# Performance work log

Measured on AMD Instinct MI355X. Metric: run time of the kernel, lower is better.

The kernel has to match this reference:

```python
import jax, jax.numpy as jnp
import numpy as np

N_NODES = 100000
N_EDGES = 1600000
IN_CH = 512
HID_CH = 256
OUT_CH = 32
K = 10


def setup_inputs() -> dict:
    key = jax.random.key(0)
    k_x, k_e, k_w1, k_b1, k_w2, k_b2 = jax.random.split(key, 6)
    x = jax.random.normal(k_x, (N_NODES, IN_CH), dtype=jnp.float32)
    edge_index = jax.random.randint(k_e, (2, N_EDGES), 0, N_NODES, dtype=jnp.int64)
    s1 = 1.0 / np.sqrt(IN_CH)
    s2 = 1.0 / np.sqrt(HID_CH)
    W1 = jax.random.uniform(k_w1, (IN_CH, HID_CH), jnp.float32, -s1, s1)
    b1 = jax.random.uniform(k_b1, (HID_CH,), jnp.float32, -s1, s1)
    W2 = jax.random.uniform(k_w2, (HID_CH, OUT_CH), jnp.float32, -s2, s2)
    b2 = jax.random.uniform(k_b2, (OUT_CH,), jnp.float32, -s2, s2)
    gamma = jnp.ones((K + 1,), jnp.float32) / (K + 1)
    return {"x": x, "edge_index": edge_index, "W1": W1, "b1": b1,
            "W2": W2, "b2": b2, "gamma": gamma}


def reference(x, edge_index, W1, b1, W2, b2, gamma):
    # MLP (dropout is identity in eval mode)
    h = jax.nn.relu(x @ W1 + b1) @ W2 + b2  # [N, out]
    row, col = edge_index[0], edge_index[1]
    # symmetric normalization: deg over destination nodes (col)
    deg = jax.ops.segment_sum(jnp.ones((N_EDGES,), h.dtype), col,
                              num_segments=N_NODES)
    deg_inv_sqrt = jnp.where(deg > 0, jax.lax.rsqrt(jnp.maximum(deg, 1.0)), 0.0)
    norm = (deg_inv_sqrt[row] * deg_inv_sqrt[col])[:, None]  # [E, 1]
    out = gamma[0] * h
    h_k = h
    for k in range(1, K + 1):
        # one hop: gather source feats, scale, scatter-add to destinations
        h_k = jax.ops.segment_sum(norm * h_k[row], col, num_segments=N_NODES)
        out = out + gamma[k] * h_k
    return out
```

## Files before the change

kernel.cpp:

```cpp
#include <hip/hip_runtime.h>
#include <hip/hip_bf16.h>

#define NN    100000
#define NE    1600000
#define INCH  512
#define HIDCH 256
#define OUTCH 32
#define KHOPS 10
#define NEPAD (NE + 3 * NN)
#define NBKT  8
#define BDIV  12500
#define BCAP  204800
#define EPB_A 8192
#define EPB_B 2048

typedef __attribute__((ext_vector_type(8))) short short8;
typedef __attribute__((ext_vector_type(4))) float f32x4;

#define GLOAD_LDS16(gsrc, ldst) \
  __builtin_amdgcn_global_load_lds((const __attribute__((address_space(1))) void*)(gsrc), \
                                   (__attribute__((address_space(3))) void*)(ldst), 16, 0, 0)

constexpr size_t ws_align(size_t x) { return (x + 255) & ~(size_t)255; }
constexpr size_t USZ = ws_align((size_t)(NN + 1) * 32 * 2);
constexpr size_t USH = USZ / 2;
constexpr size_t OFF_U0    = 0;
constexpr size_t OFF_W1TH  = OFF_U0    + 11 * USZ;
constexpr size_t OFF_W1TL  = OFF_W1TH  + ws_align((size_t)HIDCH*INCH*2);
constexpr size_t OFF_W2TH  = OFF_W1TL  + ws_align((size_t)HIDCH*INCH*2);
constexpr size_t OFF_W2TL  = OFF_W2TH  + ws_align((size_t)OUTCH*HIDCH*2);
constexpr size_t OFF_DEG   = OFF_W2TL  + ws_align((size_t)OUTCH*HIDCH*2);
constexpr size_t OFF_DIS   = OFF_DEG   + ws_align((size_t)NN*4);
constexpr size_t OFF_RP    = OFF_DIS   + ws_align((size_t)NN*4);
constexpr size_t OFF_CUR   = OFF_RP    + ws_align((size_t)(NN+1)*4);
constexpr size_t OFF_NAP   = OFF_CUR   + ws_align((size_t)NN*4);
constexpr size_t OFF_POSV  = OFF_NAP   + ws_align((size_t)NN*4);
constexpr size_t OFF_PDGP  = OFF_POSV  + ws_align((size_t)NN*4);
constexpr size_t OFF_D2P   = OFF_PDGP  + ws_align((size_t)NN*4);
constexpr size_t OFF_DSQP  = OFF_D2P   + ws_align((size_t)NN*4);
constexpr size_t OFF_CSR   = OFF_DSQP  + ws_align((size_t)NN*4);
constexpr size_t OFF_PART  = OFF_CSR   + ws_align((size_t)NEPAD*4);
constexpr size_t OFF_OFFS  = OFF_PART  + ws_align(512);
constexpr size_t OFF_BCNT  = OFF_OFFS  + ws_align(512);
constexpr size_t OFF_BINH  = OFF_BCNT  + ws_align(32);
constexpr size_t OFF_BINO  = OFF_BINH  + ws_align(256);
constexpr size_t OFF_BINC  = OFF_BINO  + ws_align(256);
constexpr size_t OFF_EPK8  = OFF_BINC  + ws_align(256);

__device__ __forceinline__ unsigned short bf16_rne(float f) {
  unsigned int u = __float_as_uint(f);
  u += 0x7fffu + ((u >> 16) & 1u);
  return (unsigned short)(u >> 16);
}
__device__ __forceinline__ float bf16_to_f32(unsigned short h) {
  return __uint_as_float(((unsigned int)h) << 16);
}
__device__ __forceinline__ float bflo(unsigned int w) {
  return __uint_as_float(w << 16);
}
__device__ __forceinline__ float bfhi(unsigned int w) {
  return __uint_as_float(w & 0xffff0000u);
}

__global__ __launch_bounds__(256) void k_bucket(const int* __restrict__ ei,
                                                int* __restrict__ deg,
                                                int* __restrict__ bcnt,
                                                int2* __restrict__ epk8) {
  __shared__ int hist[NBKT], rbase[NBKT], lcur[NBKT];
  const int t = threadIdx.x;
  const int e0 = blockIdx.x * EPB_A;
  if (t < NBKT) hist[t] = 0;
  __syncthreads();
  for (int i = t; i < EPB_A; i += 256) {
    int e = e0 + i;
    if (e < NE) {
      int c = ei[NE + e];
      atomicAdd(&deg[c], 1);
      atomicAdd(&hist[c / BDIV], 1);
    }
  }
  __syncthreads();
  if (t < NBKT) {
    rbase[t] = atomicAdd(&bcnt[t], hist[t]);
    lcur[t] = 0;
  }
  __syncthreads();
  for (int i = t; i < EPB_A; i += 256) {
    int e = e0 + i;
    if (e < NE) {
      int r = ei[e], c = ei[NE + e];
      int b = c / BDIV;
      int slot = atomicAdd(&lcur[b], 1);
      epk8[(size_t)b * BCAP + rbase[b] + slot] = make_int2(r, c);
    }
  }
}

__global__ __launch_bounds__(256) void k_dis(const int* __restrict__ deg,
                                             float* __restrict__ dis,
                                             unsigned short* __restrict__ u0,
                                             int* __restrict__ binh) {
  __shared__ int h[64];
  const int t = threadIdx.x;
  if (t < 64) h[t] = 0;
  __syncthreads();
  int v = blockIdx.x * 256 + t;
  if (v < NN) {
    int d = deg[v];
    dis[v] = d > 0 ? rsqrtf((float)d) : 0.0f;
    int bin = ((d + 3) & ~3) >> 2;
    if (bin > 63) bin = 63;
    atomicAdd(&h[bin], 1);
  }
  __syncthreads();
  if (t < 64 && h[t]) atomicAdd(&binh[t], h[t]);
  if (blockIdx.x == 0 && t < 160) {
    int tab = t >> 4, li = t & 15;
    ((unsigned int*)(u0 + (size_t)tab * USH))[(size_t)NN * 16 + li] = 0;
  }
}

__global__ __launch_bounds__(64) void k_binscan(const int* __restrict__ binh,
                                                int* __restrict__ bino,
                                                int* __restrict__ binc) {
  __shared__ int s[64];
  int t = threadIdx.x;
  int v = binh[t];
  s[t] = v;
  __syncthreads();
  for (int d = 1; d < 64; d <<= 1) {
    int x = (t >= d) ? s[t - d] : 0;
    __syncthreads();
    s[t] += x;
    __syncthreads();
  }
  bino[t] = s[t] - v;
  binc[t] = s[t] - v;
}

__global__ __launch_bounds__(256) void k_place(const int* __restrict__ deg,
                                               int* __restrict__ binc,
                                               int* __restrict__ nap,
                                               int* __restrict__ posv,
                                               int* __restrict__ pdgp) {
  __shared__ int h[64], rb[64], lc[64];
  const int t = threadIdx.x;
  if (t < 64) h[t] = 0;
  __syncthreads();
  int v = blockIdx.x * 256 + t;
  int pdeg = 0, bin = 0;
  bool valid = v < NN;
  if (valid) {
    pdeg = (deg[v] + 3) & ~3;
    bin = pdeg >> 2;
    if (bin > 63) bin = 63;
    atomicAdd(&h[bin], 1);
  }
  __syncthreads();
  if (t < 64) {
    rb[t] = h[t] ? atomicAdd(&binc[t], h[t]) : 0;
    lc[t] = 0;
  }
  __syncthreads();
  if (valid) {
    int slot = atomicAdd(&lc[bin], 1);
    int pos = rb[bin] + slot;
    nap[pos] = v;
    posv[v] = pos;
    pdgp[pos] = pdeg;
  }
}

__global__ __launch_bounds__(256) void k_scan1(const int* __restrict__ pdgp,
                                               int* __restrict__ rp,
                                               int* __restrict__ part) {
  __shared__ int s[256];
  int b = blockIdx.x, t = threadIdx.x;
  int base = b * 1024 + t * 4;
  int v0 = (base + 0 < NN) ? pdgp[base + 0] : 0;
  int v1 = (base + 1 < NN) ? pdgp[base + 1] : 0;
  int v2 = (base + 2 < NN) ? pdgp[base + 2] : 0;
  int v3 = (base + 3 < NN) ? pdgp[base + 3] : 0;
  int tot = v0 + v1 + v2 + v3;
  s[t] = tot;
  __syncthreads();
  for (int d = 1; d < 256; d <<= 1) {
    int x = (t >= d) ? s[t - d] : 0;
    __syncthreads();
    s[t] += x;
    __syncthreads();
  }
  int excl = s[t] - tot;
  if (t == 255) part[b] = s[255];
  if (base + 0 < NN) rp[base + 0] = excl;
  if (base + 1 < NN) rp[base + 1] = excl + v0;
  if (base + 2 < NN) rp[base + 2] = excl + v0 + v1;
  if (base + 3 < NN) rp[base + 3] = excl + v0 + v1 + v2;
}

__global__ __launch_bounds__(128) void k_scan2(const int* __restrict__ part,
                                               int* __restrict__ offs) {
  __shared__ int s[128];
  int t = threadIdx.x;
  int v = (t < 98) ? part[t] : 0;
  s[t] = v;
  __syncthreads();
  for (int d = 1; d < 128; d <<= 1) {
    int x = (t >= d) ? s[t - d] : 0;
    __syncthreads();
    s[t] += x;
    __syncthreads();
  }
  if (t < 98) offs[t] = s[t] - v;
}

__global__ __launch_bounds__(256) void k_scan3(int* __restrict__ rp,
                                               const int* __restrict__ offs,
                                               const int* __restrict__ part) {
  int b = blockIdx.x, t = threadIdx.x;
  int o = offs[b];
  int base = b * 1024 + t * 4;
#pragma unroll
  for (int j = 0; j < 4; ++j) {
    int i = base + j;
    if (i < NN) rp[i] += o;
  }
  if (b == 0 && t == 0) rp[NN] = offs[97] + part[97];
}

__global__ __launch_bounds__(256) void k_curinit(const int* __restrict__ nap,
                                                 const int* __restrict__ rp,
                                                 const int* __restrict__ deg,
                                                 const float* __restrict__ dis,
                                                 int* __restrict__ cur,
                                                 float* __restrict__ d2p,
                                                 float* __restrict__ dsqp) {
  int p = blockIdx.x * 256 + threadIdx.x;
  if (p < NN) {
    int v = nap[p];
    cur[v] = rp[p];
    float dv = dis[v];
    d2p[p] = dv * dv;
    int d = deg[v];
    dsqp[p] = d > 0 ? sqrtf((float)d) : 0.0f;
  }
}

__global__ __launch_bounds__(256) void k_fill2(const int2* __restrict__ epk8,
                                               const int* __restrict__ bcnt,
                                               const int* __restrict__ posv,
                                               int* __restrict__ cur,
                                               int* __restrict__ csrc) {
  const int bucket = blockIdx.x & 7;
  const int chunk = blockIdx.x >> 3;
  const int cnt = bcnt[bucket];
  const int lo = chunk * EPB_B;
  int n = cnt - lo;
  if (n > EPB_B) n = EPB_B;
  const int2* src = epk8 + (size_t)bucket * BCAP + lo;
  for (int i = threadIdx.x; i < n; i += 256) {
    int2 rc = src[i];
    int p = atomicAdd(&cur[rc.y], 1);
    csrc[p] = posv[rc.x];
  }
}

__global__ __launch_bounds__(256) void k_pad(const int* __restrict__ nap,
                                             const int* __restrict__ cur,
                                             const int* __restrict__ rp,
                                             int* __restrict__ csrc) {
  int p = blockIdx.x * 256 + threadIdx.x;
  if (p < NN) {
    int v = nap[p];
    int q = cur[v], e = rp[p + 1];
    for (; q < e; ++q) csrc[q] = NN;
  }
}

__global__ __launch_bounds__(256) void k_splitT(const float* __restrict__ src,
                                                unsigned short* __restrict__ dh,
                                                unsigned short* __restrict__ dl,
                                                int K, int N) {
  int idx = blockIdx.x * 256 + threadIdx.x;
  if (idx >= K * N) return;
  int n = idx / K, k = idx - n * K;
  float v = src[(size_t)k * N + n];
  unsigned short h = bf16_rne(v);
  dh[idx] = h;
  dl[idx] = bf16_rne(v - bf16_to_f32(h));
}

__global__ __launch_bounds__(512, 2) void k_mlp(const float* __restrict__ X,
                                                const unsigned short* __restrict__ W1Th,
                                                const float* __restrict__ bias1,
                                                const unsigned short* __restrict__ W2Th,
                                                const float* __restrict__ bias2,
                                                const float* __restrict__ gamma,
                                                const float* __restrict__ dis,
                                                const int* __restrict__ posv,
                                                unsigned short* __restrict__ u0,
                                                float* __restrict__ out) {
  __shared__ __align__(16) unsigned short Ah[2][4096];
  __shared__ __align__(16) unsigned short Bh[2][8192];
  const int t = threadIdx.x;
  const int m0 = blockIdx.x * 128;
  const int w = t >> 6, lane = t & 63;
  const int wm = w >> 2, wn = w & 3;

  const int arow = t >> 2;
  const int achk = t & 3;
  int axrow = m0 + arow; if (axrow >= NN) axrow = NN - 1;
  const float* aptr = X + (size_t)axrow * INCH + achk * 8;
  int aidx = (arow >> 4) * 512 + ((arow & 15) + achk * 16) * 8;
  aidx ^= ((aidx >> 7) & 3) << 4;
  const int aroff = (lane * 8) ^ (((lane >> 4) & 3) << 4);

  const int bn0 = (w * 16) + (lane & 15);
  const int bko = (lane >> 4) * 8;
  const unsigned short* bs0 = W1Th + (size_t)bn0 * INCH + bko;
  const unsigned short* bs1 = W1Th + (size_t)(bn0 + 128) * INCH + bko;

  f32x4 acc[4][4] = {};
  float4 av0, av1;

  av0 = *(const float4*)(aptr);
  av1 = *(const float4*)(aptr + 4);
  GLOAD_LDS16(bs0, &Bh[0][w * 512]);
  GLOAD_LDS16(bs1, &Bh[0][(w + 8) * 512]);
  {
    float af[8] = {av0.x, av0.y, av0.z, av0.w, av1.x, av1.y, av1.z, av1.w};
    short8 ah;
#pragma unroll
    for (int i = 0; i < 8; ++i) {
      unsigned int u = __float_as_uint(af[i]);
      ah[i] = (short)((u + 0x7fffu + ((u >> 16) & 1u)) >> 16);
    }
    *(short8*)&Ah[0][aidx] = ah;
  }
  __syncthreads();

#pragma unroll
  for (int it = 0; it < 16; ++it) {
    const int cur = it & 1, nxt = cur ^ 1;
    const int k0 = it * 32;
    if (it < 15) {
      av0 = *(const float4*)(aptr + k0 + 32);
      av1 = *(const float4*)(aptr + k0 + 36);
      GLOAD_LDS16(bs0 + k0 + 32, &Bh[nxt][w * 512]);
      GLOAD_LDS16(bs1 + k0 + 32, &Bh[nxt][(w + 8) * 512]);
    }
    short8 afrag[4];
#pragma unroll
    for (int mf = 0; mf < 4; ++mf)
      afrag[mf] = *(const short8*)&Ah[cur][(wm * 4 + mf) * 512 + aroff];
#pragma unroll
    for (int nf = 0; nf < 4; ++nf) {
      short8 bfh = *(const short8*)&Bh[cur][(wn * 4 + nf) * 512 + lane * 8];
#pragma unroll
      for (int mf = 0; mf < 4; ++mf) {
        acc[mf][nf] = __builtin_amdgcn_mfma_f32_16x16x32_bf16(afrag[mf], bfh, acc[mf][nf], 0, 0, 0);
      }
    }
    if (it < 15) {
      float af[8] = {av0.x, av0.y, av0.z, av0.w, av1.x, av1.y, av1.z, av1.w};
      short8 ah;
#pragma unroll
      for (int i = 0; i < 8; ++i) {
        unsigned int u = __float_as_uint(af[i]);
        ah[i] = (short)((u + 0x7fffu + ((u >> 16) & 1u)) >> 16);
      }
      *(short8*)&Ah[nxt][aidx] = ah;
    }
    __syncthreads();
  }

  unsigned short* AhF = &Ah[0][0];
  unsigned short* BhF = &Bh[0][0];

  {
#pragma unroll
    for (int q = 0; q < 2; ++q) {
      int u = w * 2 + q;
      int ngrp = u >> 3, k32 = u & 7;
      const unsigned short* src = W2Th + (size_t)(ngrp * 16 + (lane & 15)) * HIDCH
                                       + k32 * 32 + (lane >> 4) * 8;
      GLOAD_LDS16(src, &AhF[u * 512]);
    }
  }

  const int row15b = (lane >> 4) << 2;
  const int kcol = lane & 15;
  float bset[4];
#pragma unroll
  for (int nf = 0; nf < 4; ++nf) bset[nf] = bias1[wn * 64 + nf * 16 + kcol];

  if (wn < 2) {
    const int kbase = wn * 64;
#pragma unroll
    for (int nf = 0; nf < 4; ++nf) {
      int kh = kbase + nf * 16 + kcol;
      int base = ((wm * 4) * 4 + (kh >> 5)) * 512 + ((kh >> 3) & 3) * 128 + (kh & 7);
#pragma unroll
      for (int mf = 0; mf < 4; ++mf) {
#pragma unroll
        for (int r = 0; r < 4; ++r) {
          float h = fmaxf(acc[mf][nf][r] + bset[nf], 0.f);
          BhF[base + mf * 2048 + (row15b + r) * 8] = bf16_rne(h);
        }
      }
    }
  }
  __syncthreads();

  f32x4 acc2[2] = {};
#pragma unroll
  for (int s = 0; s < 4; ++s) {
    short8 a2 = *(const short8*)&BhF[(w * 4 + s) * 512 + lane * 8];
#pragma unroll
    for (int nf = 0; nf < 2; ++nf) {
      short8 bf = *(const short8*)&AhF[(nf * 8 + s) * 512 + lane * 8];
      acc2[nf] = __builtin_amdgcn_mfma_f32_16x16x32_bf16(a2, bf, acc2[nf], 0, 0, 0);
    }
  }
  __syncthreads();

  if (wn >= 2) {
    const int kbase = (wn - 2) * 64;
#pragma unroll
    for (int nf = 0; nf < 4; ++nf) {
      int kh = kbase + nf * 16 + kcol;
      int base = ((wm * 4) * 4 + (kh >> 5)) * 512 + ((kh >> 3) & 3) * 128 + (kh & 7);
#pragma unroll
      for (int mf = 0; mf < 4; ++mf) {
#pragma unroll
        for (int r = 0; r < 4; ++r) {
          float h = fmaxf(acc[mf][nf][r] + bset[nf], 0.f);
          BhF[base + mf * 2048 + (row15b + r) * 8] = bf16_rne(h);
        }
      }
    }
  }
  __syncthreads();

#pragma unroll
  for (int s = 0; s < 4; ++s) {
    short8 a2 = *(const short8*)&BhF[(w * 4 + s) * 512 + lane * 8];
#pragma unroll
    for (int nf = 0; nf < 2; ++nf) {
      short8 bf = *(const short8*)&AhF[(nf * 8 + 4 + s) * 512 + lane * 8];
      acc2[nf] = __builtin_amdgcn_mfma_f32_16x16x32_bf16(a2, bf, acc2[nf], 0, 0, 0);
    }
  }

  const float g0 = gamma[0];
  const float b2c[2] = {bias2[kcol], bias2[16 + kcol]};
#pragma unroll
  for (int nf = 0; nf < 2; ++nf) {
#pragma unroll
    for (int r = 0; r < 4; ++r) {
      int row = m0 + w * 16 + row15b + r;
      if (row < NN) {
        float h = acc2[nf][r] + b2c[nf];
        float dv = dis[row];
        size_t op = (size_t)posv[row] * 32 + nf * 16 + kcol;
        u0[op] = bf16_rne(dv * h);
        out[(size_t)row * 32 + nf * 16 + kcol] = g0 * h;
      }
    }
  }
}

__global__ __launch_bounds__(256) void k_hop(const unsigned short* __restrict__ Uin,
                                             unsigned short* __restrict__ Uout,
                                             const int* __restrict__ rp,
                                             const int* __restrict__ csrc,
                                             const float* __restrict__ d2p) {
  const int t = threadIdx.x;
  const int g = t >> 4;
  const int li = t & 15;
  const int p = blockIdx.x * 16 + g;
  const int s = rp[p], e = rp[p + 1];
  const unsigned int* Uin32 = (const unsigned int*)Uin;

  float ax0 = 0.f, ay0 = 0.f, ax1 = 0.f, ay1 = 0.f;
  float ax2 = 0.f, ay2 = 0.f, ax3 = 0.f, ay3 = 0.f;
  int j = s;
  for (; j + 8 <= e; j += 8) {
    int4 sa = *(const int4*)&csrc[j];
    int4 sb = *(const int4*)&csrc[j + 4];
    unsigned int w0 = Uin32[(size_t)sa.x * 16 + li];
    unsigned int w1 = Uin32[(size_t)sa.y * 16 + li];
    unsigned int w2 = Uin32[(size_t)sa.z * 16 + li];
    unsigned int w3 = Uin32[(size_t)sa.w * 16 + li];
    unsigned int w4 = Uin32[(size_t)sb.x * 16 + li];
    unsigned int w5 = Uin32[(size_t)sb.y * 16 + li];
    unsigned int w6 = Uin32[(size_t)sb.z * 16 + li];
    unsigned int w7 = Uin32[(size_t)sb.w * 16 + li];
    ax0 += bflo(w0); ay0 += bfhi(w0);
    ax1 += bflo(w1); ay1 += bfhi(w1);
    ax2 += bflo(w2); ay2 += bfhi(w2);
    ax3 += bflo(w3); ay3 += bfhi(w3);
    ax0 += bflo(w4); ay0 += bfhi(w4);
    ax1 += bflo(w5); ay1 += bfhi(w5);
    ax2 += bflo(w6); ay2 += bfhi(w6);
    ax3 += bflo(w7); ay3 += bfhi(w7);
  }
  if (j < e) {
    int4 sa = *(const int4*)&csrc[j];
    unsigned int w0 = Uin32[(size_t)sa.x * 16 + li];
    unsigned int w1 = Uin32[(size_t)sa.y * 16 + li];
    unsigned int w2 = Uin32[(size_t)sa.z * 16 + li];
    unsigned int w3 = Uin32[(size_t)sa.w * 16 + li];
    ax0 += bflo(w0); ay0 += bfhi(w0);
    ax1 += bflo(w1); ay1 += bfhi(w1);
    ax2 += bflo(w2); ay2 += bfhi(w2);
    ax3 += bflo(w3); ay3 += bfhi(w3);
  }
  const float Sx = (ax0 + ax1) + (ax2 + ax3);
  const float Sy = (ay0 + ay1) + (ay2 + ay3);
  const float d2 = d2p[p];
  unsigned int packed = (unsigned int)bf16_rne(d2 * Sx) |
                        ((unsigned int)bf16_rne(d2 * Sy) << 16);
  ((unsigned int*)Uout)[(size_t)p * 16 + li] = packed;
}

__global__ __launch_bounds__(256) void k_merge(const unsigned short* __restrict__ u1,
                                               const int* __restrict__ nap,
                                               const float* __restrict__ dsqp,
                                               const float* __restrict__ gamma,
                                               float* __restrict__ out) {
  const int idx = blockIdx.x * 256 + threadIdx.x;
  const int p = idx >> 4;
  const int li = idx & 15;
  const int v = nap[p];
  const float f = dsqp[p];
  const size_t o = (size_t)v * 32 + li * 2;
  float2 acc = *(const float2*)&out[o];
#pragma unroll
  for (int k = 0; k < KHOPS; ++k) {
    unsigned int w = ((const unsigned int*)(u1 + (size_t)k * USH))[(size_t)p * 16 + li];
    float gk = gamma[k + 1] * f;
    acc.x = fmaf(gk, bflo(w), acc.x);
    acc.y = fmaf(gk, bfhi(w), acc.y);
  }
  *(float2*)&out[o] = acc;
}

extern "C" void kernel_launch(void* const* d_in, const int* in_sizes, int n_in,
                              void* d_out, int out_size, void* d_ws, size_t ws_size,
                              hipStream_t stream) {
  const float* x     = (const float*)d_in[0];
  const int*   ei    = (const int*)d_in[1];
  const float* W1    = (const float*)d_in[2];
  const float* b1    = (const float*)d_in[3];
  const float* W2    = (const float*)d_in[4];
  const float* b2    = (const float*)d_in[5];
  const float* gamma = (const float*)d_in[6];
  float* out = (float*)d_out;

  char* ws = (char*)d_ws;
  unsigned short* u0   = (unsigned short*)(ws + OFF_U0);
  unsigned short* w1th = (unsigned short*)(ws + OFF_W1TH);
  unsigned short* w1tl = (unsigned short*)(ws + OFF_W1TL);
  unsigned short* w2th = (unsigned short*)(ws + OFF_W2TH);
  unsigned short* w2tl = (unsigned short*)(ws + OFF_W2TL);
  int*   deg  = (int*)(ws + OFF_DEG);
  float* dis  = (float*)(ws + OFF_DIS);
  int*   rp   = (int*)(ws + OFF_RP);
  int*   cur  = (int*)(ws + OFF_CUR);
  int*   nap  = (int*)(ws + OFF_NAP);
  int*   posv = (int*)(ws + OFF_POSV);
  int*   pdgp = (int*)(ws + OFF_PDGP);
  float* d2p  = (float*)(ws + OFF_D2P);
  float* dsqp = (float*)(ws + OFF_DSQP);
  int*   csrc = (int*)(ws + OFF_CSR);
  int*   part = (int*)(ws + OFF_PART);
  int*   offs = (int*)(ws + OFF_OFFS);
  int*   bcnt = (int*)(ws + OFF_BCNT);
  int*   binh = (int*)(ws + OFF_BINH);
  int*   bino = (int*)(ws + OFF_BINO);
  int*   binc = (int*)(ws + OFF_BINC);
  int2*  epk8 = (int2*)(ws + OFF_EPK8);

  hipMemsetAsync(deg, 0, NN * sizeof(int), stream);
  hipMemsetAsync(bcnt, 0, NBKT * sizeof(int), stream);
  hipMemsetAsync(binh, 0, 64 * sizeof(int), stream);

  k_splitT<<<(INCH * HIDCH + 255) / 256, 256, 0, stream>>>(W1, w1th, w1tl, INCH, HIDCH);
  k_splitT<<<(HIDCH * OUTCH + 255) / 256, 256, 0, stream>>>(W2, w2th, w2tl, HIDCH, OUTCH);

  k_bucket<<<(NE + EPB_A - 1) / EPB_A, 256, 0, stream>>>(ei, deg, bcnt, epk8);
  k_dis<<<(NN + 255) / 256, 256, 0, stream>>>(deg, dis, u0, binh);
  k_binscan<<<1, 64, 0, stream>>>(binh, bino, binc);
  k_place<<<(NN + 255) / 256, 256, 0, stream>>>(deg, binc, nap, posv, pdgp);
  k_scan1<<<98, 256, 0, stream>>>(pdgp, rp, part);
  k_scan2<<<1, 128, 0, stream>>>(part, offs);
  k_scan3<<<98, 256, 0, stream>>>(rp, offs, part);
  k_curinit<<<(NN + 255) / 256, 256, 0, stream>>>(nap, rp, deg, dis, cur, d2p, dsqp);
  k_fill2<<<(BCAP / EPB_B) * NBKT, 256, 0, stream>>>(epk8, bcnt, posv, cur, csrc);
  k_pad<<<(NN + 255) / 256, 256, 0, stream>>>(nap, cur, rp, csrc);

  k_mlp<<<(NN + 127) / 128, 512, 0, stream>>>(x, w1th, b1, w2th, b2, gamma, dis,
                                              posv, u0, out);

  for (int k = 1; k <= KHOPS; ++k) {
    unsigned short* uin  = u0 + (size_t)(k - 1) * USH;
    unsigned short* uout = u0 + (size_t)k * USH;
    k_hop<<<NN / 16, 256, 0, stream>>>(uin, uout, rp, csrc, d2p);
  }

  k_merge<<<NN * 16 / 256, 256, 0, stream>>>(u0 + USH, nap, dsqp, gamma, out);
}
```

Baseline: 511.7 us.

## Fuse hop propagation and merge into a single persistent cooperative kernel

Replaces the ten per-hop kernel launches and the separate merge launch with one cooperative persistent kernel. Hops are separated by grid-wide syncs, and each block walks node groups in a grid-stride loop. The aim is to remove launch gaps and tail effects between the small hop kernels. In exchange, grid.sync adds barrier cost, and the grid is capped at occupancy times 256 CUs, which may reduce the memory-level parallelism available for the gathers.

```diff
diff --git a/kernel.cpp b/kernel.cpp
--- a/kernel.cpp
+++ b/kernel.cpp
@@ -1,5 +1,8 @@
 #include <hip/hip_runtime.h>
 #include <hip/hip_bf16.h>
+#include <hip/hip_cooperative_groups.h>
+
+namespace cg = cooperative_groups;
 
 #define NN    100000
 #define NE    1600000
@@ -470,80 +473,87 @@
   }
 }
 
-__global__ __launch_bounds__(256) void k_hop(const unsigned short* __restrict__ Uin,
-                                             unsigned short* __restrict__ Uout,
-                                             const int* __restrict__ rp,
-                                             const int* __restrict__ csrc,
-                                             const float* __restrict__ d2p) {
+__global__ __launch_bounds__(256) void k_prop(unsigned short* __restrict__ u0,
+                                              const int* __restrict__ rp,
+                                              const int* __restrict__ csrc,
+                                              const float* __restrict__ d2p,
+                                              const int* __restrict__ nap,
+                                              const float* __restrict__ dsqp,
+                                              const float* __restrict__ gamma,
+                                              float* __restrict__ out) {
+  cg::grid_group grid = cg::this_grid();
   const int t = threadIdx.x;
   const int g = t >> 4;
   const int li = t & 15;
-  const int p = blockIdx.x * 16 + g;
-  const int s = rp[p], e = rp[p + 1];
-  const unsigned int* Uin32 = (const unsigned int*)Uin;
-
-  float ax0 = 0.f, ay0 = 0.f, ax1 = 0.f, ay1 = 0.f;
-  float ax2 = 0.f, ay2 = 0.f, ax3 = 0.f, ay3 = 0.f;
-  int j = s;
-  for (; j + 8 <= e; j += 8) {
-    int4 sa = *(const int4*)&csrc[j];
-    int4 sb = *(const int4*)&csrc[j + 4];
-    unsigned int w0 = Uin32[(size_t)sa.x * 16 + li];
-    unsigned int w1 = Uin32[(size_t)sa.y * 16 + li];
-    unsigned int w2 = Uin32[(size_t)sa.z * 16 + li];
-    unsigned int w3 = Uin32[(size_t)sa.w * 16 + li];
-    unsigned int w4 = Uin32[(size_t)sb.x * 16 + li];
-    unsigned int w5 = Uin32[(size_t)sb.y * 16 + li];
-    unsigned int w6 = Uin32[(size_t)sb.z * 16 + li];
-    unsigned int w7 = Uin32[(size_t)sb.w * 16 + li];
-    ax0 += bflo(w0); ay0 += bfhi(w0);
-    ax1 += bflo(w1); ay1 += bfhi(w1);
-    ax2 += bflo(w2); ay2 += bfhi(w2);
-    ax3 += bflo(w3); ay3 += bfhi(w3);
-    ax0 += bflo(w4); ay0 += bfhi(w4);
-    ax1 += bflo(w5); ay1 += bfhi(w5);
-    ax2 += bflo(w6); ay2 += bfhi(w6);
-    ax3 += bflo(w7); ay3 += bfhi(w7);
-  }
-  if (j < e) {
-    int4 sa = *(const int4*)&csrc[j];
-    unsigned int w0 = Uin32[(size_t)sa.x * 16 + li];
-    unsigned int w1 = Uin32[(size_t)sa.y * 16 + li];
-    unsigned int w2 = Uin32[(size_t)sa.z * 16 + li];
-    unsigned int w3 = Uin32[(size_t)sa.w * 16 + li];
-    ax0 += bflo(w0); ay0 += bfhi(w0);
-    ax1 += bflo(w1); ay1 += bfhi(w1);
-    ax2 += bflo(w2); ay2 += bfhi(w2);
-    ax3 += bflo(w3); ay3 += bfhi(w3);
-  }
-  const float Sx = (ax0 + ax1) + (ax2 + ax3);
-  const float Sy = (ay0 + ay1) + (ay2 + ay3);
-  const float d2 = d2p[p];
-  unsigned int packed = (unsigned int)bf16_rne(d2 * Sx) |
-                        ((unsigned int)bf16_rne(d2 * Sy) << 16);
-  ((unsigned int*)Uout)[(size_t)p * 16 + li] = packed;
-}
-
-__global__ __launch_bounds__(256) void k_merge(const unsigned short* __restrict__ u1,
-                                               const int* __restrict__ nap,
-                                               const float* __restrict__ dsqp,
-                                               const float* __restrict__ gamma,
-                                               float* __restrict__ out) {
-  const int idx = blockIdx.x * 256 + threadIdx.x;
-  const int p = idx >> 4;
-  const int li = idx & 15;
-  const int v = nap[p];
-  const float f = dsqp[p];
-  const size_t o = (size_t)v * 32 + li * 2;
-  float2 acc = *(const float2*)&out[o];
-#pragma unroll
-  for (int k = 0; k < KHOPS; ++k) {
-    unsigned int w = ((const unsigned int*)(u1 + (size_t)k * USH))[(size_t)p * 16 + li];
-    float gk = gamma[k + 1] * f;
-    acc.x = fmaf(gk, bflo(w), acc.x);
-    acc.y = fmaf(gk, bfhi(w), acc.y);
-  }
-  *(float2*)&out[o] = acc;
+  const int nwb = NN / 16;
+
+  for (int k = 1; k <= KHOPS; ++k) {
+    const unsigned int* Uin = (const unsigned int*)(u0 + (size_t)(k - 1) * USH);
+    unsigned int* Uout = (unsigned int*)(u0 + (size_t)k * USH);
+    for (int wb = blockIdx.x; wb < nwb; wb += gridDim.x) {
+      const int p = wb * 16 + g;
+      const int s = rp[p], e = rp[p + 1];
+      float ax0 = 0.f, ay0 = 0.f, ax1 = 0.f, ay1 = 0.f;
+      float ax2 = 0.f, ay2 = 0.f, ax3 = 0.f, ay3 = 0.f;
+      int j = s;
+      for (; j + 8 <= e; j += 8) {
+        int4 sa = *(const int4*)&csrc[j];
+        int4 sb = *(const int4*)&csrc[j + 4];
+        unsigned int w0 = Uin[(size_t)sa.x * 16 + li];
+        unsigned int w1 = Uin[(size_t)sa.y * 16 + li];
+        unsigned int w2 = Uin[(size_t)sa.z * 16 + li];
+        unsigned int w3 = Uin[(size_t)sa.w * 16 + li];
+        unsigned int w4 = Uin[(size_t)sb.x * 16 + li];
+        unsigned int w5 = Uin[(size_t)sb.y * 16 + li];
+        unsigned int w6 = Uin[(size_t)sb.z * 16 + li];
+        unsigned int w7 = Uin[(size_t)sb.w * 16 + li];
+        ax0 += bflo(w0); ay0 += bfhi(w0);
+        ax1 += bflo(w1); ay1 += bfhi(w1);
+        ax2 += bflo(w2); ay2 += bfhi(w2);
+        ax3 += bflo(w3); ay3 += bfhi(w3);
+        ax0 += bflo(w4); ay0 += bfhi(w4);
+        ax1 += bflo(w5); ay1 += bfhi(w5);
+        ax2 += bflo(w6); ay2 += bfhi(w6);
+        ax3 += bflo(w7); ay3 += bfhi(w7);
+      }
+      if (j < e) {
+        int4 sa = *(const int4*)&csrc[j];
+        unsigned int w0 = Uin[(size_t)sa.x * 16 + li];
+        unsigned int w1 = Uin[(size_t)sa.y * 16 + li];
+        unsigned int w2 = Uin[(size_t)sa.z * 16 + li];
+        unsigned int w3 = Uin[(size_t)sa.w * 16 + li];
+        ax0 += bflo(w0); ay0 += bfhi(w0);
+        ax1 += bflo(w1); ay1 += bfhi(w1);
+        ax2 += bflo(w2); ay2 += bfhi(w2);
+        ax3 += bflo(w3); ay3 += bfhi(w3);
+      }
+      const float Sx = (ax0 + ax1) + (ax2 + ax3);
+      const float Sy = (ay0 + ay1) + (ay2 + ay3);
+      const float d2 = d2p[p];
+      unsigned int packed = (unsigned int)bf16_rne(d2 * Sx) |
+                            ((unsigned int)bf16_rne(d2 * Sy) << 16);
+      Uout[(size_t)p * 16 + li] = packed;
+    }
+    grid.sync();
+  }
+
+  const unsigned short* u1 = u0 + USH;
+  for (int idx = blockIdx.x * 256 + t; idx < NN * 16; idx += gridDim.x * 256) {
+    const int p = idx >> 4;
+    const int li2 = idx & 15;
+    const int v = nap[p];
+    const float f = dsqp[p];
+    const size_t o = (size_t)v * 32 + li2 * 2;
+    float2 acc = *(const float2*)&out[o];
+#pragma unroll
+    for (int k = 0; k < KHOPS; ++k) {
+      unsigned int w = ((const unsigned int*)(u1 + (size_t)k * USH))[(size_t)p * 16 + li2];
+      float gk = gamma[k + 1] * f;
+      acc.x = fmaf(gk, bflo(w), acc.x);
+      acc.y = fmaf(gk, bfhi(w), acc.y);
+    }
+    *(float2*)&out[o] = acc;
+  }
 }
 
 extern "C" void kernel_launch(void* const* d_in, const int* in_sizes, int n_in,
@@ -603,11 +613,14 @@
   k_mlp<<<(NN + 127) / 128, 512, 0, stream>>>(x, w1th, b1, w2th, b2, gamma, dis,
                                               posv, u0, out);
 
-  for (int k = 1; k <= KHOPS; ++k) {
-    unsigned short* uin  = u0 + (size_t)(k - 1) * USH;
-    unsigned short* uout = u0 + (size_t)k * USH;
-    k_hop<<<NN / 16, 256, 0, stream>>>(uin, uout, rp, csrc, d2p);
-  }
-
-  k_merge<<<NN * 16 / 256, 256, 0, stream>>>(u0 + USH, nap, dsqp, gamma, out);
-}
+  int bpc = 0;
+  hipOccupancyMaxActiveBlocksPerMultiprocessor(&bpc, (const void*)k_prop, 256, 0);
+  if (bpc < 1) bpc = 1;
+  if (bpc > 8) bpc = 8;
+  int ngrid = bpc * 256;
+  if (ngrid > NN / 16) ngrid = NN / 16;
+  unsigned short* u0p = u0;
+  void* args[] = {&u0p, &rp, &csrc, &d2p, &nap, &dsqp, (void*)&gamma, (void*)&out};
+  hipLaunchCooperativeKernel((const void*)k_prop, dim3(ngrid), dim3(256),
+                             args, 0, stream);
+}
```

Result: slower. 1.797 ms (+251.1%).

## Fuse final hop with merge, unroll hop gather deeper, drop unused low-bf16 weights

Applied to the files above, without the earlier changes.

The last propagation hop is fused into the merge kernel, so the tenth hop result is consumed in registers instead of being written and reread. The hop gather loop is unrolled to 16 edges per iteration to keep more independent loads in flight. The three memsets are replaced by one zeroing kernel, and the unused low-half bf16 weight split is removed. Deeper unrolling raises register pressure and leaves a longer tail for nodes with fewer padded edges.

```diff
diff --git a/kernel.cpp b/kernel.cpp
--- a/kernel.cpp
+++ b/kernel.cpp
@@ -26,10 +26,8 @@
 constexpr size_t USH = USZ / 2;
 constexpr size_t OFF_U0    = 0;
 constexpr size_t OFF_W1TH  = OFF_U0    + 11 * USZ;
-constexpr size_t OFF_W1TL  = OFF_W1TH  + ws_align((size_t)HIDCH*INCH*2);
-constexpr size_t OFF_W2TH  = OFF_W1TL  + ws_align((size_t)HIDCH*INCH*2);
-constexpr size_t OFF_W2TL  = OFF_W2TH  + ws_align((size_t)OUTCH*HIDCH*2);
-constexpr size_t OFF_DEG   = OFF_W2TL  + ws_align((size_t)OUTCH*HIDCH*2);
+constexpr size_t OFF_W2TH  = OFF_W1TH  + ws_align((size_t)HIDCH*INCH*2);
+constexpr size_t OFF_DEG   = OFF_W2TH  + ws_align((size_t)OUTCH*HIDCH*2);
 constexpr size_t OFF_DIS   = OFF_DEG   + ws_align((size_t)NN*4);
 constexpr size_t OFF_RP    = OFF_DIS   + ws_align((size_t)NN*4);
 constexpr size_t OFF_CUR   = OFF_RP    + ws_align((size_t)(NN+1)*4);
@@ -43,8 +41,7 @@
 constexpr size_t OFF_OFFS  = OFF_PART  + ws_align(512);
 constexpr size_t OFF_BCNT  = OFF_OFFS  + ws_align(512);
 constexpr size_t OFF_BINH  = OFF_BCNT  + ws_align(32);
-constexpr size_t OFF_BINO  = OFF_BINH  + ws_align(256);
-constexpr size_t OFF_BINC  = OFF_BINO  + ws_align(256);
+constexpr size_t OFF_BINC  = OFF_BINH  + ws_align(256);
 constexpr size_t OFF_EPK8  = OFF_BINC  + ws_align(256);
 
 __device__ __forceinline__ unsigned short bf16_rne(float f) {
@@ -60,6 +57,17 @@
 }
 __device__ __forceinline__ float bfhi(unsigned int w) {
   return __uint_as_float(w & 0xffff0000u);
+}
+
+__global__ __launch_bounds__(256) void k_zero(int* __restrict__ deg,
+                                              int* __restrict__ bcnt,
+                                              int* __restrict__ binh) {
+  int i = blockIdx.x * 256 + threadIdx.x;
+  if (i < NN) deg[i] = 0;
+  if (blockIdx.x == 0) {
+    if (threadIdx.x < NBKT) bcnt[threadIdx.x] = 0;
+    if (threadIdx.x < 64) binh[threadIdx.x] = 0;
+  }
 }
 
 __global__ __launch_bounds__(256) void k_bucket(const int* __restrict__ ei,
@@ -121,7 +129,6 @@
 }
 
 __global__ __launch_bounds__(64) void k_binscan(const int* __restrict__ binh,
-                                                int* __restrict__ bino,
                                                 int* __restrict__ binc) {
   __shared__ int s[64];
   int t = threadIdx.x;
@@ -134,7 +141,6 @@
     s[t] += x;
     __syncthreads();
   }
-  bino[t] = s[t] - v;
   binc[t] = s[t] - v;
 }
 
@@ -277,17 +283,13 @@
   }
 }
 
-__global__ __launch_bounds__(256) void k_splitT(const float* __restrict__ src,
-                                                unsigned short* __restrict__ dh,
-                                                unsigned short* __restrict__ dl,
-                                                int K, int N) {
+__global__ __launch_bounds__(256) void k_cvtT(const float* __restrict__ src,
+                                              unsigned short* __restrict__ dh,
+                                              int K, int N) {
   int idx = blockIdx.x * 256 + threadIdx.x;
   if (idx >= K * N) return;
   int n = idx / K, k = idx - n * K;
-  float v = src[(size_t)k * N + n];
-  unsigned short h = bf16_rne(v);
-  dh[idx] = h;
-  dl[idx] = bf16_rne(v - bf16_to_f32(h));
+  dh[idx] = bf16_rne(src[(size_t)k * N + n]);
 }
 
 __global__ __launch_bounds__(512, 2) void k_mlp(const float* __restrict__ X,
@@ -470,6 +472,66 @@
   }
 }
 
+__device__ __forceinline__ void hop_sum(const unsigned int* __restrict__ Uin,
+                                        const int* __restrict__ csrc,
+                                        int s, int e, int li,
+                                        float& Sx, float& Sy) {
+  float ax0 = 0.f, ay0 = 0.f, ax1 = 0.f, ay1 = 0.f;
+  float ax2 = 0.f, ay2 = 0.f, ax3 = 0.f, ay3 = 0.f;
+  int j = s;
+  for (; j + 16 <= e; j += 16) {
+    int4 sa = *(const int4*)&csrc[j];
+    int4 sb = *(const int4*)&csrc[j + 4];
+    int4 sc = *(const int4*)&csrc[j + 8];
+    int4 sd = *(const int4*)&csrc[j + 12];
+    unsigned int w0 = Uin[(size_t)sa.x * 16 + li];
+    unsigned int w1 = Uin[(size_t)sa.y * 16 + li];
+    unsigned int w2 = Uin[(size_t)sa.z * 16 + li];
+    unsigned int w3 = Uin[(size_t)sa.w * 16 + li];
+    unsigned int w4 = Uin[(size_t)sb.x * 16 + li];
+    unsigned int w5 = Uin[(size_t)sb.y * 16 + li];
+    unsigned int w6 = Uin[(size_t)sb.z * 16 + li];
+    unsigned int w7 = Uin[(size_t)sb.w * 16 + li];
+    unsigned int w8 = Uin[(size_t)sc.x * 16 + li];
+    unsigned int w9 = Uin[(size_t)sc.y * 16 + li];
+    unsigned int wa = Uin[(size_t)sc.z * 16 + li];
+    unsigned int wb = Uin[(size_t)sc.w * 16 + li];
+    unsigned int wc = Uin[(size_t)sd.x * 16 + li];
+    unsigned int wd = Uin[(size_t)sd.y * 16 + li];
+    unsigned int we = Uin[(size_t)sd.z * 16 + li];
+    unsigned int wf = Uin[(size_t)sd.w * 16 + li];
+    ax0 += bflo(w0); ay0 += bfhi(w0);
+    ax1 += bflo(w1); ay1 += bfhi(w1);
+    ax2 += bflo(w2); ay2 += bfhi(w2);
+    ax3 += bflo(w3); ay3 += bfhi(w3);
+    ax0 += bflo(w4); ay0 += bfhi(w4);
+    ax1 += bflo(w5); ay1 += bfhi(w5);
+    ax2 += bflo(w6); ay2 += bfhi(w6);
+    ax3 += bflo(w7); ay3 += bfhi(w7);
+    ax0 += bflo(w8); ay0 += bfhi(w8);
+    ax1 += bflo(w9); ay1 += bfhi(w9);
+    ax2 += bflo(wa); ay2 += bfhi(wa);
+    ax3 += bflo(wb); ay3 += bfhi(wb);
+    ax0 += bflo(wc); ay0 += bfhi(wc);
+    ax1 += bflo(wd); ay1 += bfhi(wd);
+    ax2 += bflo(we); ay2 += bfhi(we);
+    ax3 += bflo(wf); ay3 += bfhi(wf);
+  }
+  for (; j + 4 <= e; j += 4) {
+    int4 sa = *(const int4*)&csrc[j];
+    unsigned int w0 = Uin[(size_t)sa.x * 16 + li];
+    unsigned int w1 = Uin[(size_t)sa.y * 16 + li];
+    unsigned int w2 = Uin[(size_t)sa.z * 16 + li];
+    unsigned int w3 = Uin[(size_t)sa.w * 16 + li];
+    ax0 += bflo(w0); ay0 += bfhi(w0);
+    ax1 += bflo(w1); ay1 += bfhi(w1);
+    ax2 += bflo(w2); ay2 += bfhi(w2);
+    ax3 += bflo(w3); ay3 += bfhi(w3);
+  }
+  Sx = (ax0 + ax1) + (ax2 + ax3);
+  Sy = (ay0 + ay1) + (ay2 + ay3);
+}
+
 __global__ __launch_bounds__(256) void k_hop(const unsigned short* __restrict__ Uin,
                                              unsigned short* __restrict__ Uout,
                                              const int* __restrict__ rp,
@@ -480,69 +542,47 @@
   const int li = t & 15;
   const int p = blockIdx.x * 16 + g;
   const int s = rp[p], e = rp[p + 1];
-  const unsigned int* Uin32 = (const unsigned int*)Uin;
-
-  float ax0 = 0.f, ay0 = 0.f, ax1 = 0.f, ay1 = 0.f;
-  float ax2 = 0.f, ay2 = 0.f, ax3 = 0.f, ay3 = 0.f;
-  int j = s;
-  for (; j + 8 <= e; j += 8) {
-    int4 sa = *(const int4*)&csrc[j];
-    int4 sb = *(const int4*)&csrc[j + 4];
-    unsigned int w0 = Uin32[(size_t)sa.x * 16 + li];
-    unsigned int w1 = Uin32[(size_t)sa.y * 16 + li];
-    unsigned int w2 = Uin32[(size_t)sa.z * 16 + li];
-    unsigned int w3 = Uin32[(size_t)sa.w * 16 + li];
-    unsigned int w4 = Uin32[(size_t)sb.x * 16 + li];
-    unsigned int w5 = Uin32[(size_t)sb.y * 16 + li];
-    unsigned int w6 = Uin32[(size_t)sb.z * 16 + li];
-    unsigned int w7 = Uin32[(size_t)sb.w * 16 + li];
-    ax0 += bflo(w0); ay0 += bfhi(w0);
-    ax1 += bflo(w1); ay1 += bfhi(w1);
-    ax2 += bflo(w2); ay2 += bfhi(w2);
-    ax3 += bflo(w3); ay3 += bfhi(w3);
-    ax0 += bflo(w4); ay0 += bfhi(w4);
-    ax1 += bflo(w5); ay1 += bfhi(w5);
-    ax2 += bflo(w6); ay2 += bfhi(w6);
-    ax3 += bflo(w7); ay3 += bfhi(w7);
-  }
-  if (j < e) {
-    int4 sa = *(const int4*)&csrc[j];
-    unsigned int w0 = Uin32[(size_t)sa.x * 16 + li];
-    unsigned int w1 = Uin32[(size_t)sa.y * 16 + li];
-    unsigned int w2 = Uin32[(size_t)sa.z * 16 + li];
-    unsigned int w3 = Uin32[(size_t)sa.w * 16 + li];
-    ax0 += bflo(w0); ay0 += bfhi(w0);
-    ax1 += bflo(w1); ay1 += bfhi(w1);
-    ax2 += bflo(w2); ay2 += bfhi(w2);
-    ax3 += bflo(w3); ay3 += bfhi(w3);
-  }
-  const float Sx = (ax0 + ax1) + (ax2 + ax3);
-  const float Sy = (ay0 + ay1) + (ay2 + ay3);
+  float Sx, Sy;
+  hop_sum((const unsigned int*)Uin, csrc, s, e, li, Sx, Sy);
   const float d2 = d2p[p];
   unsigned int packed = (unsigned int)bf16_rne(d2 * Sx) |
                         ((unsigned int)bf16_rne(d2 * Sy) << 16);
   ((unsigned int*)Uout)[(size_t)p * 16 + li] = packed;
 }
 
-__global__ __launch_bounds__(256) void k_merge(const unsigned short* __restrict__ u1,
-                                               const int* __restrict__ nap,
-                                               const float* __restrict__ dsqp,
-                                               const float* __restrict__ gamma,
-                                               float* __restrict__ out) {
-  const int idx = blockIdx.x * 256 + threadIdx.x;
-  const int p = idx >> 4;
-  const int li = idx & 15;
+__global__ __launch_bounds__(256) void k_hop_last(const unsigned short* __restrict__ u0,
+                                                  const int* __restrict__ rp,
+                                                  const int* __restrict__ csrc,
+                                                  const float* __restrict__ d2p,
+                                                  const int* __restrict__ nap,
+                                                  const float* __restrict__ dsqp,
+                                                  const float* __restrict__ gamma,
+                                                  float* __restrict__ out) {
+  const int t = threadIdx.x;
+  const int g = t >> 4;
+  const int li = t & 15;
+  const int p = blockIdx.x * 16 + g;
+  const int s = rp[p], e = rp[p + 1];
+  const unsigned short* u9 = u0 + (size_t)(KHOPS - 1) * USH;
+  float Sx, Sy;
+  hop_sum((const unsigned int*)u9, csrc, s, e, li, Sx, Sy);
+  const float d2 = d2p[p];
+  const float u10x = d2 * Sx, u10y = d2 * Sy;
+
   const int v = nap[p];
   const float f = dsqp[p];
   const size_t o = (size_t)v * 32 + li * 2;
   float2 acc = *(const float2*)&out[o];
 #pragma unroll
-  for (int k = 0; k < KHOPS; ++k) {
-    unsigned int w = ((const unsigned int*)(u1 + (size_t)k * USH))[(size_t)p * 16 + li];
-    float gk = gamma[k + 1] * f;
+  for (int k = 1; k < KHOPS; ++k) {
+    unsigned int w = ((const unsigned int*)(u0 + (size_t)k * USH))[(size_t)p * 16 + li];
+    float gk = gamma[k] * f;
     acc.x = fmaf(gk, bflo(w), acc.x);
     acc.y = fmaf(gk, bfhi(w), acc.y);
   }
+  const float g10 = gamma[KHOPS] * f;
+  acc.x = fmaf(g10, u10x, acc.x);
+  acc.y = fmaf(g10, u10y, acc.y);
   *(float2*)&out[o] = acc;
 }
 
@@ -561,9 +601,7 @@
   char* ws = (char*)d_ws;
   unsigned short* u0   = (unsigned short*)(ws + OFF_U0);
   unsigned short* w1th = (unsigned short*)(ws + OFF_W1TH);
-  unsigned short* w1tl = (unsigned short*)(ws + OFF_W1TL);
   unsigned short* w2th = (unsigned short*)(ws + OFF_W2TH);
-  unsigned short* w2tl = (unsigned short*)(ws + OFF_W2TL);
   int*   deg  = (int*)(ws + OFF_DEG);
   float* dis  = (float*)(ws + OFF_DIS);
   int*   rp   = (int*)(ws + OFF_RP);
@@ -578,20 +616,17 @@
   int*   offs = (int*)(ws + OFF_OFFS);
   int*   bcnt = (int*)(ws + OFF_BCNT);
   int*   binh = (int*)(ws + OFF_BINH);
-  int*   bino = (int*)(ws + OFF_BINO);
   int*   binc = (int*)(ws + OFF_BINC);
   int2*  epk8 = (int2*)(ws + OFF_EPK8);
 
-  hipMemsetAsync(deg, 0, NN * sizeof(int), stream);
-  hipMemsetAsync(bcnt, 0, NBKT * sizeof(int), stream);
-  hipMemsetAsync(binh, 0, 64 * sizeof(int), stream);
-
-  k_splitT<<<(INCH * HIDCH + 255) / 256, 256, 0, stream>>>(W1, w1th, w1tl, INCH, HIDCH);
-  k_splitT<<<(HIDCH * OUTCH + 255) / 256, 256, 0, stream>>>(W2, w2th, w2tl, HIDCH, OUTCH);
+  k_zero<<<(NN + 255) / 256, 256, 0, stream>>>(deg, bcnt, binh);
+
+  k_cvtT<<<(INCH * HIDCH + 255) / 256, 256, 0, stream>>>(W1, w1th, INCH, HIDCH);
+  k_cvtT<<<(HIDCH * OUTCH + 255) / 256, 256, 0, stream>>>(W2, w2th, HIDCH, OUTCH);
 
   k_bucket<<<(NE + EPB_A - 1) / EPB_A, 256, 0, stream>>>(ei, deg, bcnt, epk8);
   k_dis<<<(NN + 255) / 256, 256, 0, stream>>>(deg, dis, u0, binh);
-  k_binscan<<<1, 64, 0, stream>>>(binh, bino, binc);
+  k_binscan<<<1, 64, 0, stream>>>(binh, binc);
   k_place<<<(NN + 255) / 256, 256, 0, stream>>>(deg, binc, nap, posv, pdgp);
   k_scan1<<<98, 256, 0, stream>>>(pdgp, rp, part);
   k_scan2<<<1, 128, 0, stream>>>(part, offs);
@@ -603,11 +638,10 @@
   k_mlp<<<(NN + 127) / 128, 512, 0, stream>>>(x, w1th, b1, w2th, b2, gamma, dis,
                                               posv, u0, out);
 
-  for (int k = 1; k <= KHOPS; ++k) {
+  for (int k = 1; k < KHOPS; ++k) {
     unsigned short* uin  = u0 + (size_t)(k - 1) * USH;
     unsigned short* uout = u0 + (size_t)k * USH;
     k_hop<<<NN / 16, 256, 0, stream>>>(uin, uout, rp, csrc, d2p);
   }
-
-  k_merge<<<NN * 16 / 256, 256, 0, stream>>>(u0 + USH, nap, dsqp, gamma, out);
-}
+  k_hop_last<<<NN / 16, 256, 0, stream>>>(u0, rp, csrc, d2p, nap, dsqp, gamma, out);
+}
```

After: 510.5 us. About the same (-0.2%).
